# Kernel optimization log

Measured on AMD Instinct MI355X. Metric: run time of the kernel, lower is better.

Reference implementation:

```python
import jax, jax.numpy as jnp
import numpy as np

CAPACITY_FACTOR = 1.25
TOP_K = 2


def setup_inputs() -> dict:
    key = jax.random.key(0)
    ks = jax.random.split(key, 4)
    B, T, D, H, N = 8, 8192, 512, 512, 32
    x = jax.random.normal(ks[0], (B, T, D), jnp.float32)
    Wg = jax.random.normal(ks[1], (D, N), jnp.float32) * 0.02   # gate (no bias)
    W1 = jax.random.normal(ks[2], (N, D, H), jnp.float32) * 0.02  # stacked expert fc1
    b1 = jnp.zeros((N, H), jnp.float32)
    W2 = jax.random.normal(ks[3], (N, H, D), jnp.float32) * 0.02  # stacked expert fc2
    b2 = jnp.zeros((N, D), jnp.float32)
    return {"x": x, "Wg": Wg, "W1": W1, "b1": b1, "W2": W2, "b2": b2}


def _moe(x, Wg, W1, b1, W2, b2):
    B, T, D = x.shape
    N = Wg.shape[1]
    K = TOP_K
    BT = B * T
    BTK = BT * K
    C = int(np.ceil(CAPACITY_FACTOR * BTK / N))  # capacity per expert (static)

    x_flat = x.reshape(BT, D)
    probs = jax.nn.softmax(x_flat @ Wg, axis=-1)            # [BT, N]
    vals, idx = jax.lax.top_k(probs, K)                     # [BT, K]
    vals = vals / jnp.clip(vals.sum(-1, keepdims=True), 1e-9)  # normalize_gates

    # Assignments in the exact order of the original double loop: pos-major, j-minor.
    a = idx.reshape(BTK)                                    # expert id per assignment
    oh = jax.nn.one_hot(a, N, dtype=jnp.int32)              # [BTK, N]
    rank = jnp.cumsum(oh, axis=0) - oh                      # prior count for each expert
    pos = jnp.take_along_axis(rank, a[:, None], axis=1)[:, 0]  # slot within expert
    keep = pos < C                                          # capacity-limited dispatch
    dest = jnp.where(keep, a * C + pos, N * C)              # OOB sentinel -> dropped
    token = jnp.arange(BTK) // K                            # source token per assignment

    # Dispatch: scatter kept tokens into per-expert capacity buffers [N, C, D].
    buf = jnp.zeros((N * C, D), x.dtype).at[dest].set(x_flat[token], mode="drop")
    buf = buf.reshape(N, C, D)

    # Expert FFN (grouped GEMMs). FeedForwardExpert assumed Linear-ReLU-Linear.
    h = jax.nn.relu(jnp.einsum("ncd,ndh->nch", buf, W1) + b1[:, None, :])
    o = (jnp.einsum("nch,nhd->ncd", h, W2) + b2[:, None, :]).reshape(N * C, D)

    # Combine: gather expert outputs, weight by gates, scatter-add back by token.
    gathered = o[jnp.minimum(dest, N * C - 1)]              # dropped rows zeroed via w
    w = vals.reshape(BTK) * keep.astype(x.dtype)
    y_flat = jax.ops.segment_sum(gathered * w[:, None], token, num_segments=BT)
    contrib = jax.ops.segment_sum(w, token, num_segments=BT)
    # Tokens with no surviving assignment pass through unchanged.
    y_flat = jnp.where(contrib[:, None] <= 1e-12, x_flat, y_flat)
    return y_flat.reshape(B, T, D)


def reference(x, Wg, W1, b1, W2, b2):
    return _moe(x, Wg, W1, b1, W2, b2)
```

## Files before the change

### kernel.cpp

```cpp
#include <hip/hip_runtime.h>
#include <hip/hip_bf16.h>

#define BT 65536
#define DD 512
#define HH 512
#define NE 32
#define CAP 5120
#define BM 64
#define NRB 80

typedef float  f32x4  __attribute__((ext_vector_type(4)));
typedef short  bf16x8 __attribute__((ext_vector_type(8)));

__device__ __forceinline__ unsigned short f2bf(float f){
    unsigned int u = __builtin_bit_cast(unsigned int, f);
    unsigned int r = (u + 0x7fffu + ((u >> 16) & 1u)) >> 16;
    return (unsigned short)r;
}
__device__ __forceinline__ float bf2f(unsigned short h){
    unsigned int u = ((unsigned int)h) << 16;
    return __builtin_bit_cast(float, u);
}

__global__ __launch_bounds__(256) void k_wgprep(
    const float* __restrict__ Wg,
    unsigned short* __restrict__ WgHf, unsigned short* __restrict__ WgLf)
{
    int entry = blockIdx.x * 256 + threadIdx.x;
    int ln = entry & 63;
    unsigned short h[8], l[8];
    #pragma unroll
    for (int j = 0; j < 8; j++){
        int d = ((entry >> 6) & 15)*32 + (ln >> 4)*8 + j;
        int e = (entry >> 10)*16 + (ln & 15);
        float v = Wg[d*NE + e];
        unsigned short hi = f2bf(v);
        h[j] = hi;
        l[j] = f2bf(v - bf2f(hi));
    }
    *(bf16x8*)(WgHf + (size_t)entry*8) = *(bf16x8*)h;
    *(bf16x8*)(WgLf + (size_t)entry*8) = *(bf16x8*)l;
}

__global__ __launch_bounds__(256) void k_prep(
    const float* __restrict__ x, const float* __restrict__ Wg,
    const float* __restrict__ W1, const float* __restrict__ W2,
    const unsigned short* __restrict__ WgHf, const unsigned short* __restrict__ WgLf,
    unsigned short* __restrict__ W1f, unsigned short* __restrict__ W2f,
    int* __restrict__ counts, int* __restrict__ gsl, float* __restrict__ wts,
    unsigned char* __restrict__ flags, unsigned short* __restrict__ xb16)
{
    __shared__ float lg2[64 * 33];
    __shared__ int lcnt[NE], lbase[NE];

    int tid = threadIdx.x;

    if (blockIdx.x >= 1024){
        int b = blockIdx.x - 1024;
        int w = b >> 8;
        int e = (b >> 3) & 31;
        int kq = b & 7;
        const float* src = (w ? W2 : W1) + ((size_t)e << 18);
        unsigned short* dst = (w ? W2f : W1f) + ((size_t)e << 18);
        int n4 = (tid & 127) * 4;
        int kh = tid >> 7;
        #pragma unroll 1
        for (int kg = 0; kg < 4; kg++){
            int k0 = kq*64 + (kg*2 + kh)*8;
            float4 rows[8];
            #pragma unroll
            for (int j = 0; j < 8; j++)
                rows[j] = *(const float4*)&src[(size_t)(k0 + j)*512 + n4];
            unsigned short v0[8], v1[8], v2[8], v3[8];
            #pragma unroll
            for (int j = 0; j < 8; j++){
                v0[j] = f2bf(rows[j].x); v1[j] = f2bf(rows[j].y);
                v2[j] = f2bf(rows[j].z); v3[j] = f2bf(rows[j].w);
            }
            int kc = k0 >> 5, lb = ((k0 >> 3) & 3)*16;
            #pragma unroll
            for (int m = 0; m < 4; m++){
                int n = n4 + m;
                int nt = n >> 4, ln = lb + (n & 15);
                const unsigned short* vv = (m==0)?v0:(m==1)?v1:(m==2)?v2:v3;
                *(bf16x8*)(dst + (((size_t)(nt*16 + kc)*64 + ln) << 3)) = *(const bf16x8*)vv;
            }
        }
        return;
    }

    int t0 = blockIdx.x * 64;
    {
        int lane = tid & 63;
        int wv   = tid >> 6;
        int lg   = lane >> 4, ll = lane & 15;
        int tokl = wv*16 + ll;
        const float* xr = x + (size_t)(t0 + tokl)*DD;

        f32x4 acc0 = (f32x4)0.f, acc1 = (f32x4)0.f;
        #pragma unroll 4
        for (int kc = 0; kc < 16; kc++){
            int d0 = kc*32 + lg*8;
            float4 a = *(const float4*)(xr + d0);
            float4 b = *(const float4*)(xr + d0 + 4);
            unsigned short h[8], l[8];
            h[0]=f2bf(a.x); h[1]=f2bf(a.y); h[2]=f2bf(a.z); h[3]=f2bf(a.w);
            h[4]=f2bf(b.x); h[5]=f2bf(b.y); h[6]=f2bf(b.z); h[7]=f2bf(b.w);
            l[0]=f2bf(a.x-bf2f(h[0])); l[1]=f2bf(a.y-bf2f(h[1]));
            l[2]=f2bf(a.z-bf2f(h[2])); l[3]=f2bf(a.w-bf2f(h[3]));
            l[4]=f2bf(b.x-bf2f(h[4])); l[5]=f2bf(b.y-bf2f(h[5]));
            l[6]=f2bf(b.z-bf2f(h[6])); l[7]=f2bf(b.w-bf2f(h[7]));
            bf16x8 bh = *(bf16x8*)h, bl = *(bf16x8*)l;
            *(bf16x8*)(xb16 + (size_t)(t0 + tokl)*DD + d0) = bh;
            bf16x8 ah0 = *(const bf16x8*)(WgHf + ((size_t)(kc*64 + lane) << 3));
            bf16x8 al0 = *(const bf16x8*)(WgLf + ((size_t)(kc*64 + lane) << 3));
            bf16x8 ah1 = *(const bf16x8*)(WgHf + ((size_t)(1024 + kc*64 + lane) << 3));
            bf16x8 al1 = *(const bf16x8*)(WgLf + ((size_t)(1024 + kc*64 + lane) << 3));
            acc0 = __builtin_amdgcn_mfma_f32_16x16x32_bf16(ah0, bh, acc0, 0, 0, 0);
            acc0 = __builtin_amdgcn_mfma_f32_16x16x32_bf16(ah0, bl, acc0, 0, 0, 0);
            acc0 = __builtin_amdgcn_mfma_f32_16x16x32_bf16(al0, bh, acc0, 0, 0, 0);
            acc1 = __builtin_amdgcn_mfma_f32_16x16x32_bf16(ah1, bh, acc1, 0, 0, 0);
            acc1 = __builtin_amdgcn_mfma_f32_16x16x32_bf16(ah1, bl, acc1, 0, 0, 0);
            acc1 = __builtin_amdgcn_mfma_f32_16x16x32_bf16(al1, bh, acc1, 0, 0, 0);
        }
        #pragma unroll
        for (int i = 0; i < 4; i++){
            lg2[tokl*33 +      lg*4 + i] = acc0[i];
            lg2[tokl*33 + 16 + lg*4 + i] = acc1[i];
        }
    }
    if (tid < NE) lcnt[tid] = 0;
    __syncthreads();

    float w1 = 0.f, w2 = 0.f;
    int i1 = 0, i2 = 0, s1 = 0, s2 = 0;
    bool act = (tid < 64);
    if (act){
        int tok = t0 + tid;
        float acc[NE];
        #pragma unroll
        for (int n = 0; n < NE; n++) acc[n] = lg2[tid*33 + n];

        float v1 = -1e30f; i1 = -1;
        #pragma unroll
        for (int n = 0; n < NE; n++) if (acc[n] > v1){ v1 = acc[n]; i1 = n; }
        float v2 = -1e30f; i2 = -1;
        #pragma unroll
        for (int n = 0; n < NE; n++) if (n != i1 && acc[n] > v2){ v2 = acc[n]; i2 = n; }
        float v3 = -1e30f;
        #pragma unroll
        for (int n = 0; n < NE; n++) if (n != i1 && n != i2 && acc[n] > v3) v3 = acc[n];

        if (v2 - v3 >= 1e-4f){
            double ex  = exp((double)v2 - (double)v1);
            double inv = 1.0 / (1.0 + ex);
            w1 = (float)inv; w2 = (float)(ex * inv);
        } else {
            const float* xr = x + (size_t)tok * DD;
            float thresh = v2 - 1e-3f;
            unsigned cmask = 0u;
            #pragma unroll
            for (int n = 0; n < NE; n++) cmask |= (acc[n] >= thresh) ? (1u << n) : 0u;
            double dv1 = -1.0e300, dv2 = -1.0e300; int di1 = -1, di2 = -1;
            #pragma unroll 1
            for (int n = 0; n < NE; n++){
                if (!((cmask >> n) & 1u)) continue;
                double q0 = 0.0, q1 = 0.0, q2 = 0.0, q3 = 0.0;
                #pragma unroll 4
                for (int d = 0; d < DD; d += 4){
                    q0 = fma((double)xr[d+0], (double)Wg[(size_t)(d+0)*NE + n], q0);
                    q1 = fma((double)xr[d+1], (double)Wg[(size_t)(d+1)*NE + n], q1);
                    q2 = fma((double)xr[d+2], (double)Wg[(size_t)(d+2)*NE + n], q2);
                    q3 = fma((double)xr[d+3], (double)Wg[(size_t)(d+3)*NE + n], q3);
                }
                double sv = (q0 + q1) + (q2 + q3);
                if (sv > dv1){ dv2 = dv1; di2 = di1; dv1 = sv; di1 = n; }
                else if (sv > dv2){ dv2 = sv; di2 = n; }
            }
            i1 = di1; i2 = di2;
            double ex  = exp(dv2 - dv1);
            double inv = 1.0 / (1.0 + ex);
            w1 = (float)inv; w2 = (float)(ex * inv);
        }
        s1 = atomicAdd(&lcnt[i1], 1);
        s2 = atomicAdd(&lcnt[i2], 1);
    }
    __syncthreads();
    if (tid < NE && lcnt[tid] > 0) lbase[tid] = atomicAdd(&counts[tid], lcnt[tid]);
    __syncthreads();
    if (act){
        int tok = t0 + tid;
        int g1 = lbase[i1] + s1;
        int g2 = lbase[i2] + s2;
        bool k1 = g1 < CAP, k2 = g2 < CAP;
        if (k1){ gsl[i1*CAP + g1] = tok;               wts[i1*CAP + g1] = w1; }
        if (k2){ gsl[i2*CAP + g2] = tok | (1 << 20);   wts[i2*CAP + g2] = w2; }
        flags[tok] = (unsigned char)((k1 ? 1 : 0) | (k2 ? 2 : 0));
    }
}

__global__ __launch_bounds__(512, 4) void k_ffn(
    const unsigned short* __restrict__ xb16,
    const unsigned short* __restrict__ W1f,
    const unsigned short* __restrict__ W2f,
    const float* __restrict__ b1, const float* __restrict__ b2,
    const int* __restrict__ counts,
    const int* __restrict__ gsl, const float* __restrict__ wts,
    float* __restrict__ y, unsigned short* __restrict__ y2h)
{
    __shared__ unsigned char AH[64 * 1024];

    int p  = blockIdx.x;
    int s  = p >> 3;
    int e  = ((s / NRB) << 3) | (p & 7);
    int rb = s % NRB;

    int cnt = counts[e]; if (cnt > CAP) cnt = CAP;
    int r0 = rb * BM;
    if (r0 >= cnt) return;

    int tid  = threadIdx.x;
    int lane = tid & 63;
    int wv   = tid >> 6;
    int lg   = lane >> 4;
    int ll   = lane & 15;

    {
        int row = tid >> 3, seg = tid & 7;
        int gr  = r0 + row;
        char* rowb = (char*)AH + row * 1024;
        int rsw = (row & 7) << 4;
        if (gr < cnt){
            int tk = gsl[e*CAP + gr] & 0xFFFFF;
            const uint4* src = (const uint4*)(xb16 + (size_t)tk*DD + seg*64);
            #pragma unroll
            for (int j = 0; j < 8; j++){
                uint4 v = src[j];
                int chunk = seg*8 + j;
                *(uint4*)(rowb + ((chunk << 4) ^ rsw)) = v;
            }
        } else {
            uint4 zz; zz.x = zz.y = zz.z = zz.w = 0u;
            #pragma unroll
            for (int j = 0; j < 8; j++){
                int chunk = seg*8 + j;
                *(uint4*)(rowb + ((chunk << 4) ^ rsw)) = zz;
            }
        }
    }
    __syncthreads();

    f32x4 acc[4][4];
    #pragma unroll
    for (int a2 = 0; a2 < 4; a2++)
        #pragma unroll
        for (int tt = 0; tt < 4; tt++)
            acc[a2][tt] = (f32x4)0.f;

    {
        const unsigned short* Wa = W1f + ((size_t)e << 18) + (size_t)wv*32768;
        bf16x8 f0[4], f1[4];
        #pragma unroll
        for (int a2 = 0; a2 < 4; a2++)
            f0[a2] = *(const bf16x8*)(Wa + a2*8192 + lane*8);
        #pragma unroll 1
        for (int c = 0; c < 16; c += 2){
            #pragma unroll
            for (int a2 = 0; a2 < 4; a2++)
                f1[a2] = *(const bf16x8*)(Wa + a2*8192 + (c+1)*512 + lane*8);
            {
                bf16x8 bx[4];
                #pragma unroll
                for (int tt = 0; tt < 4; tt++){
                    int tok = tt*16 + ll;
                    int bofs = (64*c + 16*lg) ^ ((tok & 7) << 4);
                    bx[tt] = *(const bf16x8*)((char*)AH + tok*1024 + bofs);
                }
                __builtin_amdgcn_s_setprio(1);
                #pragma unroll
                for (int a2 = 0; a2 < 4; a2++)
                    #pragma unroll
                    for (int tt = 0; tt < 4; tt++)
                        acc[a2][tt] = __builtin_amdgcn_mfma_f32_16x16x32_bf16(f0[a2], bx[tt], acc[a2][tt], 0, 0, 0);
                __builtin_amdgcn_s_setprio(0);
            }
            if (c + 2 < 16){
                #pragma unroll
                for (int a2 = 0; a2 < 4; a2++)
                    f0[a2] = *(const bf16x8*)(Wa + a2*8192 + (c+2)*512 + lane*8);
            }
            {
                bf16x8 bx[4];
                #pragma unroll
                for (int tt = 0; tt < 4; tt++){
                    int tok = tt*16 + ll;
                    int bofs = (64*(c+1) + 16*lg) ^ ((tok & 7) << 4);
                    bx[tt] = *(const bf16x8*)((char*)AH + tok*1024 + bofs);
                }
                __builtin_amdgcn_s_setprio(1);
                #pragma unroll
                for (int a2 = 0; a2 < 4; a2++)
                    #pragma unroll
                    for (int tt = 0; tt < 4; tt++)
                        acc[a2][tt] = __builtin_amdgcn_mfma_f32_16x16x32_bf16(f1[a2], bx[tt], acc[a2][tt], 0, 0, 0);
                __builtin_amdgcn_s_setprio(0);
            }
        }
    }
    __syncthreads();

    #pragma unroll
    for (int a2 = 0; a2 < 4; a2++){
        int n0 = wv*64 + a2*16 + lg*4;
        float4 bv = *(const float4*)(b1 + e*HH + n0);
        #pragma unroll
        for (int tt = 0; tt < 4; tt++){
            int tok = tt*16 + ll;
            float h0 = acc[a2][tt][0] + bv.x; h0 = h0 > 0.f ? h0 : 0.f;
            float h1 = acc[a2][tt][1] + bv.y; h1 = h1 > 0.f ? h1 : 0.f;
            float h2 = acc[a2][tt][2] + bv.z; h2 = h2 > 0.f ? h2 : 0.f;
            float h3 = acc[a2][tt][3] + bv.w; h3 = h3 > 0.f ? h3 : 0.f;
            uint2 pk;
            pk.x = (unsigned)f2bf(h0) | ((unsigned)f2bf(h1) << 16);
            pk.y = (unsigned)f2bf(h2) | ((unsigned)f2bf(h3) << 16);
            int bofs = (n0*2) ^ ((tok & 7) << 4);
            *(uint2*)((char*)AH + tok*1024 + bofs) = pk;
            acc[a2][tt] = (f32x4)0.f;
        }
    }
    __syncthreads();

    {
        const unsigned short* Wb = W2f + ((size_t)e << 18) + (size_t)wv*32768;
        bf16x8 f0[4], f1[4];
        #pragma unroll
        for (int b_ = 0; b_ < 4; b_++)
            f0[b_] = *(const bf16x8*)(Wb + b_*8192 + lane*8);
        #pragma unroll 1
        for (int kc = 0; kc < 16; kc += 2){
            #pragma unroll
            for (int b_ = 0; b_ < 4; b_++)
                f1[b_] = *(const bf16x8*)(Wb + b_*8192 + (kc+1)*512 + lane*8);
            {
                bf16x8 ah[4];
                #pragma unroll
                for (int tt = 0; tt < 4; tt++){
                    int tok = tt*16 + ll;
                    int bofs = (64*kc + 16*lg) ^ ((tok & 7) << 4);
                    ah[tt] = *(const bf16x8*)((char*)AH + tok*1024 + bofs);
                }
                __builtin_amdgcn_s_setprio(1);
                #pragma unroll
                for (int b_ = 0; b_ < 4; b_++)
                    #pragma unroll
                    for (int tt = 0; tt < 4; tt++)
                        acc[b_][tt] = __builtin_amdgcn_mfma_f32_16x16x32_bf16(ah[tt], f0[b_], acc[b_][tt], 0, 0, 0);
                __builtin_amdgcn_s_setprio(0);
            }
            if (kc + 2 < 16){
                #pragma unroll
                for (int b_ = 0; b_ < 4; b_++)
                    f0[b_] = *(const bf16x8*)(Wb + b_*8192 + (kc+2)*512 + lane*8);
            }
            {
                bf16x8 ah[4];
                #pragma unroll
                for (int tt = 0; tt < 4; tt++){
                    int tok = tt*16 + ll;
                    int bofs = (64*(kc+1) + 16*lg) ^ ((tok & 7) << 4);
                    ah[tt] = *(const bf16x8*)((char*)AH + tok*1024 + bofs);
                }
                __builtin_amdgcn_s_setprio(1);
                #pragma unroll
                for (int b_ = 0; b_ < 4; b_++)
                    #pragma unroll
                    for (int tt = 0; tt < 4; tt++)
                        acc[b_][tt] = __builtin_amdgcn_mfma_f32_16x16x32_bf16(ah[tt], f1[b_], acc[b_][tt], 0, 0, 0);
                __builtin_amdgcn_s_setprio(0);
            }
        }
    }

    float bb[4];
    #pragma unroll
    for (int b_ = 0; b_ < 4; b_++)
        bb[b_] = b2[e*DD + wv*64 + b_*16 + ll];

    #pragma unroll
    for (int tt = 0; tt < 4; tt++){
        #pragma unroll
        for (int i = 0; i < 4; i++){
            int rl = tt*16 + lg*4 + i;
            int gr = r0 + rl;
            if (gr < cnt){
                int   v  = gsl[e*CAP + gr];
                int   tk = v & 0xFFFFF;
                float w  = wts[e*CAP + gr];
                if (v >> 20){
                    unsigned short* dst = y2h + (size_t)tk * DD;
                    #pragma unroll
                    for (int b_ = 0; b_ < 4; b_++){
                        int col = wv*64 + b_*16 + ll;
                        dst[col] = f2bf(w * (acc[b_][tt][i] + bb[b_]));
                    }
                } else {
                    float* dst = y + (size_t)tk * DD;
                    #pragma unroll
                    for (int b_ = 0; b_ < 4; b_++){
                        int col = wv*64 + b_*16 + ll;
                        dst[col] = w * (acc[b_][tt][i] + bb[b_]);
                    }
                }
            }
        }
    }
}

__global__ __launch_bounds__(256) void k_comb(
    const float* __restrict__ x, const unsigned short* __restrict__ y2h,
    const unsigned char* __restrict__ flags, float* __restrict__ y)
{
    const float4* x4  = (const float4*)x;
    const uint2*  y24 = (const uint2*)y2h;
    float4* y4 = (float4*)y;
    int nthreads = gridDim.x * 256;
    int g = blockIdx.x * 256 + threadIdx.x;
    #pragma unroll 1
    for (long long idx = g; idx < (long long)BT * 128; idx += nthreads){
        int t = (int)(idx >> 7);
        int f = flags[t];
        if (f == 3){
            float4 a = y4[idx];
            uint2 p = y24[idx];
            a.x += bf2f((unsigned short)(p.x & 0xFFFF));
            a.y += bf2f((unsigned short)(p.x >> 16));
            a.z += bf2f((unsigned short)(p.y & 0xFFFF));
            a.w += bf2f((unsigned short)(p.y >> 16));
            y4[idx] = a;
        } else if (f == 2){
            uint2 p = y24[idx];
            float4 a;
            a.x = bf2f((unsigned short)(p.x & 0xFFFF));
            a.y = bf2f((unsigned short)(p.x >> 16));
            a.z = bf2f((unsigned short)(p.y & 0xFFFF));
            a.w = bf2f((unsigned short)(p.y >> 16));
            y4[idx] = a;
        } else if (f == 0){
            y4[idx] = x4[idx];
        }
    }
}

extern "C" void kernel_launch(void* const* d_in, const int* in_sizes, int n_in,
                              void* d_out, int out_size, void* d_ws, size_t ws_size,
                              hipStream_t stream)
{
    const float* x  = (const float*)d_in[0];
    const float* Wg = (const float*)d_in[1];
    const float* W1 = (const float*)d_in[2];
    const float* b1 = (const float*)d_in[3];
    const float* W2 = (const float*)d_in[4];
    const float* b2 = (const float*)d_in[5];
    float* y = (float*)d_out;

    char* ws = (char*)d_ws;
    unsigned short* W1f = (unsigned short*)(ws);
    unsigned short* W2f = (unsigned short*)(ws + 16777216);
    size_t b3 = 33554432;
    int*   counts = (int*)  (ws + b3);
    int*   gsl    = (int*)  (ws + b3 + 256);
    float* wts    = (float*)(ws + b3 + 256 + 655360);
    unsigned char* flags = (unsigned char*)(ws + b3 + 256 + 2*655360);
    unsigned short* WgHf = (unsigned short*)(ws + b3 + 256 + 2*655360 + 65536);
    unsigned short* WgLf = (unsigned short*)(ws + b3 + 256 + 2*655360 + 65536 + 32768);
    unsigned short* xb16 = (unsigned short*)(ws + 35651584);
    unsigned short* y2h  = (unsigned short*)(ws + 35651584 + 67108864);

    hipMemsetAsync(counts, 0, 256, stream);
    hipLaunchKernelGGL(k_wgprep, dim3(8), dim3(256), 0, stream, Wg, WgHf, WgLf);
    hipLaunchKernelGGL(k_prep, dim3(1024 + 512), dim3(256), 0, stream,
                       x, Wg, W1, W2, WgHf, WgLf, W1f, W2f, counts, gsl, wts, flags, xb16);
    hipLaunchKernelGGL(k_ffn,  dim3(NE*NRB), dim3(512), 0, stream,
                       xb16, W1f, W2f, b1, b2, counts, gsl, wts, y, y2h);
    hipLaunchKernelGGL(k_comb, dim3(2048), dim3(256), 0, stream, x, y2h, flags, y);
}
```

Measured before the change: 356.1 us.

## Split prep into conversion and gating kernels; deepen FFN weight prefetch pipeline

The combined prep kernel is split in two. A conversion kernel casts the expert weights and the x-to-bf16 copy, and a separate gating kernel handles routing only, so the gate loop no longer stores xb16. In the FFN kernel the weight fragments are now prefetched four k-chunks ahead in named registers instead of double-buffered one step ahead, and launch bounds drop from 4 to 3 waves per SIMD to make room for the larger register budget. The deeper prefetch is meant to hide global-load latency behind MFMA work. The costs are one extra kernel launch, an extra full read of x, and lower occupancy.

Measured after the change: 444.5 us. +24.8%, slower.

```diff
diff --git a/kernel.cpp b/kernel.cpp
--- a/kernel.cpp
+++ b/kernel.cpp
@@ -42,21 +42,15 @@
     *(bf16x8*)(WgLf + (size_t)entry*8) = *(bf16x8*)l;
 }
 
-__global__ __launch_bounds__(256) void k_prep(
-    const float* __restrict__ x, const float* __restrict__ Wg,
+__global__ __launch_bounds__(256) void k_conv(
+    const float* __restrict__ x,
     const float* __restrict__ W1, const float* __restrict__ W2,
-    const unsigned short* __restrict__ WgHf, const unsigned short* __restrict__ WgLf,
     unsigned short* __restrict__ W1f, unsigned short* __restrict__ W2f,
-    int* __restrict__ counts, int* __restrict__ gsl, float* __restrict__ wts,
-    unsigned char* __restrict__ flags, unsigned short* __restrict__ xb16)
-{
-    __shared__ float lg2[64 * 33];
-    __shared__ int lcnt[NE], lbase[NE];
-
+    unsigned short* __restrict__ xb16)
+{
     int tid = threadIdx.x;
-
-    if (blockIdx.x >= 1024){
-        int b = blockIdx.x - 1024;
+    if (blockIdx.x < 512){
+        int b = blockIdx.x;
         int w = b >> 8;
         int e = (b >> 3) & 31;
         int kq = b & 7;
@@ -86,9 +80,34 @@
                 *(bf16x8*)(dst + (((size_t)(nt*16 + kc)*64 + ln) << 3)) = *(const bf16x8*)vv;
             }
         }
-        return;
-    }
-
+    } else {
+        int b = blockIdx.x - 512;
+        size_t base = (size_t)b * 65536;
+        const float* xs = x + base;
+        unsigned short* xd = xb16 + base;
+        #pragma unroll 1
+        for (int i = 0; i < 32; i++){
+            int o = (i*256 + tid)*8;
+            float4 a = *(const float4*)(xs + o);
+            float4 c = *(const float4*)(xs + o + 4);
+            bf16x8 pk;
+            pk[0]=(short)f2bf(a.x); pk[1]=(short)f2bf(a.y); pk[2]=(short)f2bf(a.z); pk[3]=(short)f2bf(a.w);
+            pk[4]=(short)f2bf(c.x); pk[5]=(short)f2bf(c.y); pk[6]=(short)f2bf(c.z); pk[7]=(short)f2bf(c.w);
+            *(bf16x8*)(xd + o) = pk;
+        }
+    }
+}
+
+__global__ __launch_bounds__(256) void k_gate(
+    const float* __restrict__ x, const float* __restrict__ Wg,
+    const unsigned short* __restrict__ WgHf, const unsigned short* __restrict__ WgLf,
+    int* __restrict__ counts, int* __restrict__ gsl, float* __restrict__ wts,
+    unsigned char* __restrict__ flags)
+{
+    __shared__ float lg2[64 * 33];
+    __shared__ int lcnt[NE], lbase[NE];
+
+    int tid = threadIdx.x;
     int t0 = blockIdx.x * 64;
     {
         int lane = tid & 63;
@@ -111,7 +130,6 @@
             l[4]=f2bf(b.x-bf2f(h[4])); l[5]=f2bf(b.y-bf2f(h[5]));
             l[6]=f2bf(b.z-bf2f(h[6])); l[7]=f2bf(b.w-bf2f(h[7]));
             bf16x8 bh = *(bf16x8*)h, bl = *(bf16x8*)l;
-            *(bf16x8*)(xb16 + (size_t)(t0 + tokl)*DD + d0) = bh;
             bf16x8 ah0 = *(const bf16x8*)(WgHf + ((size_t)(kc*64 + lane) << 3));
             bf16x8 al0 = *(const bf16x8*)(WgLf + ((size_t)(kc*64 + lane) << 3));
             bf16x8 ah1 = *(const bf16x8*)(WgHf + ((size_t)(1024 + kc*64 + lane) << 3));
@@ -199,7 +217,63 @@
     }
 }
 
-__global__ __launch_bounds__(512, 4) void k_ffn(
+#define LW(A,B,C,D,P,CC) { \
+    A = *(const bf16x8*)((P) + (CC)*512 + lane*8); \
+    B = *(const bf16x8*)((P) + 8192 + (CC)*512 + lane*8); \
+    C = *(const bf16x8*)((P) + 16384 + (CC)*512 + lane*8); \
+    D = *(const bf16x8*)((P) + 24576 + (CC)*512 + lane*8); }
+
+#define CHUNK1(CC,A,B,C,D) { \
+    int base_ = (64*(CC) + 16*lg) ^ sw_; \
+    bf16x8 x0_ = *(const bf16x8*)((char*)AH + (ll)*1024      + base_); \
+    bf16x8 x1_ = *(const bf16x8*)((char*)AH + (16+ll)*1024   + base_); \
+    bf16x8 x2_ = *(const bf16x8*)((char*)AH + (32+ll)*1024   + base_); \
+    bf16x8 x3_ = *(const bf16x8*)((char*)AH + (48+ll)*1024   + base_); \
+    __builtin_amdgcn_s_setprio(1); \
+    acc[0][0]=__builtin_amdgcn_mfma_f32_16x16x32_bf16(A,x0_,acc[0][0],0,0,0); \
+    acc[0][1]=__builtin_amdgcn_mfma_f32_16x16x32_bf16(A,x1_,acc[0][1],0,0,0); \
+    acc[0][2]=__builtin_amdgcn_mfma_f32_16x16x32_bf16(A,x2_,acc[0][2],0,0,0); \
+    acc[0][3]=__builtin_amdgcn_mfma_f32_16x16x32_bf16(A,x3_,acc[0][3],0,0,0); \
+    acc[1][0]=__builtin_amdgcn_mfma_f32_16x16x32_bf16(B,x0_,acc[1][0],0,0,0); \
+    acc[1][1]=__builtin_amdgcn_mfma_f32_16x16x32_bf16(B,x1_,acc[1][1],0,0,0); \
+    acc[1][2]=__builtin_amdgcn_mfma_f32_16x16x32_bf16(B,x2_,acc[1][2],0,0,0); \
+    acc[1][3]=__builtin_amdgcn_mfma_f32_16x16x32_bf16(B,x3_,acc[1][3],0,0,0); \
+    acc[2][0]=__builtin_amdgcn_mfma_f32_16x16x32_bf16(C,x0_,acc[2][0],0,0,0); \
+    acc[2][1]=__builtin_amdgcn_mfma_f32_16x16x32_bf16(C,x1_,acc[2][1],0,0,0); \
+    acc[2][2]=__builtin_amdgcn_mfma_f32_16x16x32_bf16(C,x2_,acc[2][2],0,0,0); \
+    acc[2][3]=__builtin_amdgcn_mfma_f32_16x16x32_bf16(C,x3_,acc[2][3],0,0,0); \
+    acc[3][0]=__builtin_amdgcn_mfma_f32_16x16x32_bf16(D,x0_,acc[3][0],0,0,0); \
+    acc[3][1]=__builtin_amdgcn_mfma_f32_16x16x32_bf16(D,x1_,acc[3][1],0,0,0); \
+    acc[3][2]=__builtin_amdgcn_mfma_f32_16x16x32_bf16(D,x2_,acc[3][2],0,0,0); \
+    acc[3][3]=__builtin_amdgcn_mfma_f32_16x16x32_bf16(D,x3_,acc[3][3],0,0,0); \
+    __builtin_amdgcn_s_setprio(0); }
+
+#define CHUNK2(CC,A,B,C,D) { \
+    int base_ = (64*(CC) + 16*lg) ^ sw_; \
+    bf16x8 x0_ = *(const bf16x8*)((char*)AH + (ll)*1024      + base_); \
+    bf16x8 x1_ = *(const bf16x8*)((char*)AH + (16+ll)*1024   + base_); \
+    bf16x8 x2_ = *(const bf16x8*)((char*)AH + (32+ll)*1024   + base_); \
+    bf16x8 x3_ = *(const bf16x8*)((char*)AH + (48+ll)*1024   + base_); \
+    __builtin_amdgcn_s_setprio(1); \
+    acc[0][0]=__builtin_amdgcn_mfma_f32_16x16x32_bf16(x0_,A,acc[0][0],0,0,0); \
+    acc[0][1]=__builtin_amdgcn_mfma_f32_16x16x32_bf16(x1_,A,acc[0][1],0,0,0); \
+    acc[0][2]=__builtin_amdgcn_mfma_f32_16x16x32_bf16(x2_,A,acc[0][2],0,0,0); \
+    acc[0][3]=__builtin_amdgcn_mfma_f32_16x16x32_bf16(x3_,A,acc[0][3],0,0,0); \
+    acc[1][0]=__builtin_amdgcn_mfma_f32_16x16x32_bf16(x0_,B,acc[1][0],0,0,0); \
+    acc[1][1]=__builtin_amdgcn_mfma_f32_16x16x32_bf16(x1_,B,acc[1][1],0,0,0); \
+    acc[1][2]=__builtin_amdgcn_mfma_f32_16x16x32_bf16(x2_,B,acc[1][2],0,0,0); \
+    acc[1][3]=__builtin_amdgcn_mfma_f32_16x16x32_bf16(x3_,B,acc[1][3],0,0,0); \
+    acc[2][0]=__builtin_amdgcn_mfma_f32_16x16x32_bf16(x0_,C,acc[2][0],0,0,0); \
+    acc[2][1]=__builtin_amdgcn_mfma_f32_16x16x32_bf16(x1_,C,acc[2][1],0,0,0); \
+    acc[2][2]=__builtin_amdgcn_mfma_f32_16x16x32_bf16(x2_,C,acc[2][2],0,0,0); \
+    acc[2][3]=__builtin_amdgcn_mfma_f32_16x16x32_bf16(x3_,C,acc[2][3],0,0,0); \
+    acc[3][0]=__builtin_amdgcn_mfma_f32_16x16x32_bf16(x0_,D,acc[3][0],0,0,0); \
+    acc[3][1]=__builtin_amdgcn_mfma_f32_16x16x32_bf16(x1_,D,acc[3][1],0,0,0); \
+    acc[3][2]=__builtin_amdgcn_mfma_f32_16x16x32_bf16(x2_,D,acc[3][2],0,0,0); \
+    acc[3][3]=__builtin_amdgcn_mfma_f32_16x16x32_bf16(x3_,D,acc[3][3],0,0,0); \
+    __builtin_amdgcn_s_setprio(0); }
+
+__global__ __launch_bounds__(512, 3) void k_ffn(
     const unsigned short* __restrict__ xb16,
     const unsigned short* __restrict__ W1f,
     const unsigned short* __restrict__ W2f,
@@ -224,6 +298,7 @@
     int wv   = tid >> 6;
     int lg   = lane >> 4;
     int ll   = lane & 15;
+    int sw_  = (ll & 7) << 4;
 
     {
         int row = tid >> 3, seg = tid & 7;
@@ -259,52 +334,21 @@
 
     {
         const unsigned short* Wa = W1f + ((size_t)e << 18) + (size_t)wv*32768;
-        bf16x8 f0[4], f1[4];
-        #pragma unroll
-        for (int a2 = 0; a2 < 4; a2++)
-            f0[a2] = *(const bf16x8*)(Wa + a2*8192 + lane*8);
+        bf16x8 q0a,q0b,q0c,q0d, q1a,q1b,q1c,q1d, q2a,q2b,q2c,q2d, q3a,q3b,q3c,q3d;
+        LW(q0a,q0b,q0c,q0d,Wa,0)
+        LW(q1a,q1b,q1c,q1d,Wa,1)
+        LW(q2a,q2b,q2c,q2d,Wa,2)
+        LW(q3a,q3b,q3c,q3d,Wa,3)
         #pragma unroll 1
-        for (int c = 0; c < 16; c += 2){
-            #pragma unroll
-            for (int a2 = 0; a2 < 4; a2++)
-                f1[a2] = *(const bf16x8*)(Wa + a2*8192 + (c+1)*512 + lane*8);
-            {
-                bf16x8 bx[4];
-                #pragma unroll
-                for (int tt = 0; tt < 4; tt++){
-                    int tok = tt*16 + ll;
-                    int bofs = (64*c + 16*lg) ^ ((tok & 7) << 4);
-                    bx[tt] = *(const bf16x8*)((char*)AH + tok*1024 + bofs);
-                }
-                __builtin_amdgcn_s_setprio(1);
-                #pragma unroll
-                for (int a2 = 0; a2 < 4; a2++)
-                    #pragma unroll
-                    for (int tt = 0; tt < 4; tt++)
-                        acc[a2][tt] = __builtin_amdgcn_mfma_f32_16x16x32_bf16(f0[a2], bx[tt], acc[a2][tt], 0, 0, 0);
-                __builtin_amdgcn_s_setprio(0);
-            }
-            if (c + 2 < 16){
-                #pragma unroll
-                for (int a2 = 0; a2 < 4; a2++)
-                    f0[a2] = *(const bf16x8*)(Wa + a2*8192 + (c+2)*512 + lane*8);
-            }
-            {
-                bf16x8 bx[4];
-                #pragma unroll
-                for (int tt = 0; tt < 4; tt++){
-                    int tok = tt*16 + ll;
-                    int bofs = (64*(c+1) + 16*lg) ^ ((tok & 7) << 4);
-                    bx[tt] = *(const bf16x8*)((char*)AH + tok*1024 + bofs);
-                }
-                __builtin_amdgcn_s_setprio(1);
-                #pragma unroll
-                for (int a2 = 0; a2 < 4; a2++)
-                    #pragma unroll
-                    for (int tt = 0; tt < 4; tt++)
-                        acc[a2][tt] = __builtin_amdgcn_mfma_f32_16x16x32_bf16(f1[a2], bx[tt], acc[a2][tt], 0, 0, 0);
-                __builtin_amdgcn_s_setprio(0);
-            }
+        for (int c = 0; c < 16; c += 4){
+            CHUNK1(c,   q0a,q0b,q0c,q0d)
+            if (c+4 < 16) LW(q0a,q0b,q0c,q0d,Wa,c+4)
+            CHUNK1(c+1, q1a,q1b,q1c,q1d)
+            if (c+5 < 16) LW(q1a,q1b,q1c,q1d,Wa,c+5)
+            CHUNK1(c+2, q2a,q2b,q2c,q2d)
+            if (c+6 < 16) LW(q2a,q2b,q2c,q2d,Wa,c+6)
+            CHUNK1(c+3, q3a,q3b,q3c,q3d)
+            if (c+7 < 16) LW(q3a,q3b,q3c,q3d,Wa,c+7)
         }
     }
     __syncthreads();
@@ -332,52 +376,21 @@
 
     {
         const unsigned short* Wb = W2f + ((size_t)e << 18) + (size_t)wv*32768;
-        bf16x8 f0[4], f1[4];
-        #pragma unroll
-        for (int b_ = 0; b_ < 4; b_++)
-            f0[b_] = *(const bf16x8*)(Wb + b_*8192 + lane*8);
+        bf16x8 q0a,q0b,q0c,q0d, q1a,q1b,q1c,q1d, q2a,q2b,q2c,q2d, q3a,q3b,q3c,q3d;
+        LW(q0a,q0b,q0c,q0d,Wb,0)
+        LW(q1a,q1b,q1c,q1d,Wb,1)
+        LW(q2a,q2b,q2c,q2d,Wb,2)
+        LW(q3a,q3b,q3c,q3d,Wb,3)
         #pragma unroll 1
-        for (int kc = 0; kc < 16; kc += 2){
-            #pragma unroll
-            for (int b_ = 0; b_ < 4; b_++)
-                f1[b_] = *(const bf16x8*)(Wb + b_*8192 + (kc+1)*512 + lane*8);
-            {
-                bf16x8 ah[4];
-                #pragma unroll
-                for (int tt = 0; tt < 4; tt++){
-                    int tok = tt*16 + ll;
-                    int bofs = (64*kc + 16*lg) ^ ((tok & 7) << 4);
-                    ah[tt] = *(const bf16x8*)((char*)AH + tok*1024 + bofs);
-                }
-                __builtin_amdgcn_s_setprio(1);
-                #pragma unroll
-                for (int b_ = 0; b_ < 4; b_++)
-                    #pragma unroll
-                    for (int tt = 0; tt < 4; tt++)
-                        acc[b_][tt] = __builtin_amdgcn_mfma_f32_16x16x32_bf16(ah[tt], f0[b_], acc[b_][tt], 0, 0, 0);
-                __builtin_amdgcn_s_setprio(0);
-            }
-            if (kc + 2 < 16){
-                #pragma unroll
-                for (int b_ = 0; b_ < 4; b_++)
-                    f0[b_] = *(const bf16x8*)(Wb + b_*8192 + (kc+2)*512 + lane*8);
-            }
-            {
-                bf16x8 ah[4];
-                #pragma unroll
-                for (int tt = 0; tt < 4; tt++){
-                    int tok = tt*16 + ll;
-                    int bofs = (64*(kc+1) + 16*lg) ^ ((tok & 7) << 4);
-                    ah[tt] = *(const bf16x8*)((char*)AH + tok*1024 + bofs);
-                }
-                __builtin_amdgcn_s_setprio(1);
-                #pragma unroll
-                for (int b_ = 0; b_ < 4; b_++)
-                    #pragma unroll
-                    for (int tt = 0; tt < 4; tt++)
-                        acc[b_][tt] = __builtin_amdgcn_mfma_f32_16x16x32_bf16(ah[tt], f1[b_], acc[b_][tt], 0, 0, 0);
-                __builtin_amdgcn_s_setprio(0);
-            }
+        for (int kc = 0; kc < 16; kc += 4){
+            CHUNK2(kc,   q0a,q0b,q0c,q0d)
+            if (kc+4 < 16) LW(q0a,q0b,q0c,q0d,Wb,kc+4)
+            CHUNK2(kc+1, q1a,q1b,q1c,q1d)
+            if (kc+5 < 16) LW(q1a,q1b,q1c,q1d,Wb,kc+5)
+            CHUNK2(kc+2, q2a,q2b,q2c,q2d)
+            if (kc+6 < 16) LW(q2a,q2b,q2c,q2d,Wb,kc+6)
+            CHUNK2(kc+3, q3a,q3b,q3c,q3d)
+            if (kc+7 < 16) LW(q3a,q3b,q3c,q3d,Wb,kc+7)
         }
     }
 
@@ -478,9 +491,8 @@
 
     hipMemsetAsync(counts, 0, 256, stream);
     hipLaunchKernelGGL(k_wgprep, dim3(8), dim3(256), 0, stream, Wg, WgHf, WgLf);
-    hipLaunchKernelGGL(k_prep, dim3(1024 + 512), dim3(256), 0, stream,
-                       x, Wg, W1, W2, WgHf, WgLf, W1f, W2f, counts, gsl, wts, flags, xb16);
-    hipLaunchKernelGGL(k_ffn,  dim3(NE*NRB), dim3(512), 0, stream,
-                       xb16, W1f, W2f, b1, b2, counts, gsl, wts, y, y2h);
+    hipLaunchKernelGGL(k_conv, dim3(1024), dim3(256), 0, stream, x, W1, W2, W1f, W2f, xb16);
+    hipLaunchKernelGGL(k_gate, dim3(BT/64), dim3(256), 0, stream, x, Wg, WgHf, WgLf, counts, gsl, wts, flags);
+    hipLaunchKernelGGL(k_ffn,  dim3(NE*NRB), dim3(512), 0, stream, xb16, W1f, W2f, b1, b2, counts, gsl, wts, y, y2h);
     hipLaunchKernelGGL(k_comb, dim3(2048), dim3(256), 0, stream, x, y2h, flags, y);
 }
```

## Split prep kernel, prefetch gate loads, write both expert outputs as bf16

Applied to the files above, without the earlier changes.

The combined prep kernel is split into a weight-conversion kernel and a gating kernel. The gate loop now prefetches the next x chunk one iteration ahead. The FFN writes the first-choice contribution to a bf16 scratch buffer instead of directly into fp32 y, and the combine kernel sums both bf16 buffers. This aims to cut scattered fp32 write traffic and hide load latency, at the cost of an extra launch, an extra buffer read in combine, and lower precision for the first-choice output.

Result: no change. 362.8 us (+1.9%).

```diff
diff --git a/kernel.cpp b/kernel.cpp
--- a/kernel.cpp
+++ b/kernel.cpp
@@ -42,11 +42,46 @@
     *(bf16x8*)(WgLf + (size_t)entry*8) = *(bf16x8*)l;
 }
 
-__global__ __launch_bounds__(256) void k_prep(
+__global__ __launch_bounds__(256) void k_wconv(
+    const float* __restrict__ W1, const float* __restrict__ W2,
+    unsigned short* __restrict__ W1f, unsigned short* __restrict__ W2f)
+{
+    int tid = threadIdx.x;
+    int b = blockIdx.x;
+    int w = b >> 8;
+    int e = (b >> 3) & 31;
+    int kq = b & 7;
+    const float* src = (w ? W2 : W1) + ((size_t)e << 18);
+    unsigned short* dst = (w ? W2f : W1f) + ((size_t)e << 18);
+    int n4 = (tid & 127) * 4;
+    int kh = tid >> 7;
+    #pragma unroll 1
+    for (int kg = 0; kg < 4; kg++){
+        int k0 = kq*64 + (kg*2 + kh)*8;
+        float4 rows[8];
+        #pragma unroll
+        for (int j = 0; j < 8; j++)
+            rows[j] = *(const float4*)&src[(size_t)(k0 + j)*512 + n4];
+        unsigned short v0[8], v1[8], v2[8], v3[8];
+        #pragma unroll
+        for (int j = 0; j < 8; j++){
+            v0[j] = f2bf(rows[j].x); v1[j] = f2bf(rows[j].y);
+            v2[j] = f2bf(rows[j].z); v3[j] = f2bf(rows[j].w);
+        }
+        int kc = k0 >> 5, lb = ((k0 >> 3) & 3)*16;
+        #pragma unroll
+        for (int m = 0; m < 4; m++){
+            int n = n4 + m;
+            int nt = n >> 4, ln = lb + (n & 15);
+            const unsigned short* vv = (m==0)?v0:(m==1)?v1:(m==2)?v2:v3;
+            *(bf16x8*)(dst + (((size_t)(nt*16 + kc)*64 + ln) << 3)) = *(const bf16x8*)vv;
+        }
+    }
+}
+
+__global__ __launch_bounds__(256) void k_gate(
     const float* __restrict__ x, const float* __restrict__ Wg,
-    const float* __restrict__ W1, const float* __restrict__ W2,
     const unsigned short* __restrict__ WgHf, const unsigned short* __restrict__ WgLf,
-    unsigned short* __restrict__ W1f, unsigned short* __restrict__ W2f,
     int* __restrict__ counts, int* __restrict__ gsl, float* __restrict__ wts,
     unsigned char* __restrict__ flags, unsigned short* __restrict__ xb16)
 {
@@ -54,41 +89,6 @@
     __shared__ int lcnt[NE], lbase[NE];
 
     int tid = threadIdx.x;
-
-    if (blockIdx.x >= 1024){
-        int b = blockIdx.x - 1024;
-        int w = b >> 8;
-        int e = (b >> 3) & 31;
-        int kq = b & 7;
-        const float* src = (w ? W2 : W1) + ((size_t)e << 18);
-        unsigned short* dst = (w ? W2f : W1f) + ((size_t)e << 18);
-        int n4 = (tid & 127) * 4;
-        int kh = tid >> 7;
-        #pragma unroll 1
-        for (int kg = 0; kg < 4; kg++){
-            int k0 = kq*64 + (kg*2 + kh)*8;
-            float4 rows[8];
-            #pragma unroll
-            for (int j = 0; j < 8; j++)
-                rows[j] = *(const float4*)&src[(size_t)(k0 + j)*512 + n4];
-            unsigned short v0[8], v1[8], v2[8], v3[8];
-            #pragma unroll
-            for (int j = 0; j < 8; j++){
-                v0[j] = f2bf(rows[j].x); v1[j] = f2bf(rows[j].y);
-                v2[j] = f2bf(rows[j].z); v3[j] = f2bf(rows[j].w);
-            }
-            int kc = k0 >> 5, lb = ((k0 >> 3) & 3)*16;
-            #pragma unroll
-            for (int m = 0; m < 4; m++){
-                int n = n4 + m;
-                int nt = n >> 4, ln = lb + (n & 15);
-                const unsigned short* vv = (m==0)?v0:(m==1)?v1:(m==2)?v2:v3;
-                *(bf16x8*)(dst + (((size_t)(nt*16 + kc)*64 + ln) << 3)) = *(const bf16x8*)vv;
-            }
-        }
-        return;
-    }
-
     int t0 = blockIdx.x * 64;
     {
         int lane = tid & 63;
@@ -98,11 +98,14 @@
         const float* xr = x + (size_t)(t0 + tokl)*DD;
 
         f32x4 acc0 = (f32x4)0.f, acc1 = (f32x4)0.f;
+        float4 pa = *(const float4*)(xr + lg*8);
+        float4 pb = *(const float4*)(xr + lg*8 + 4);
         #pragma unroll 4
         for (int kc = 0; kc < 16; kc++){
-            int d0 = kc*32 + lg*8;
-            float4 a = *(const float4*)(xr + d0);
-            float4 b = *(const float4*)(xr + d0 + 4);
+            int dn = (kc < 15) ? (kc+1)*32 + lg*8 : lg*8;
+            float4 na = *(const float4*)(xr + dn);
+            float4 nb = *(const float4*)(xr + dn + 4);
+            float4 a = pa, b = pb;
             unsigned short h[8], l[8];
             h[0]=f2bf(a.x); h[1]=f2bf(a.y); h[2]=f2bf(a.z); h[3]=f2bf(a.w);
             h[4]=f2bf(b.x); h[5]=f2bf(b.y); h[6]=f2bf(b.z); h[7]=f2bf(b.w);
@@ -111,7 +114,7 @@
             l[4]=f2bf(b.x-bf2f(h[4])); l[5]=f2bf(b.y-bf2f(h[5]));
             l[6]=f2bf(b.z-bf2f(h[6])); l[7]=f2bf(b.w-bf2f(h[7]));
             bf16x8 bh = *(bf16x8*)h, bl = *(bf16x8*)l;
-            *(bf16x8*)(xb16 + (size_t)(t0 + tokl)*DD + d0) = bh;
+            *(bf16x8*)(xb16 + (size_t)(t0 + tokl)*DD + kc*32 + lg*8) = bh;
             bf16x8 ah0 = *(const bf16x8*)(WgHf + ((size_t)(kc*64 + lane) << 3));
             bf16x8 al0 = *(const bf16x8*)(WgLf + ((size_t)(kc*64 + lane) << 3));
             bf16x8 ah1 = *(const bf16x8*)(WgHf + ((size_t)(1024 + kc*64 + lane) << 3));
@@ -122,6 +125,7 @@
             acc1 = __builtin_amdgcn_mfma_f32_16x16x32_bf16(ah1, bh, acc1, 0, 0, 0);
             acc1 = __builtin_amdgcn_mfma_f32_16x16x32_bf16(ah1, bl, acc1, 0, 0, 0);
             acc1 = __builtin_amdgcn_mfma_f32_16x16x32_bf16(al1, bh, acc1, 0, 0, 0);
+            pa = na; pb = nb;
         }
         #pragma unroll
         for (int i = 0; i < 4; i++){
@@ -206,7 +210,7 @@
     const float* __restrict__ b1, const float* __restrict__ b2,
     const int* __restrict__ counts,
     const int* __restrict__ gsl, const float* __restrict__ wts,
-    float* __restrict__ y, unsigned short* __restrict__ y2h)
+    unsigned short* __restrict__ y1h, unsigned short* __restrict__ y2h)
 {
     __shared__ unsigned char AH[64 * 1024];
 
@@ -396,20 +400,11 @@
                 int   v  = gsl[e*CAP + gr];
                 int   tk = v & 0xFFFFF;
                 float w  = wts[e*CAP + gr];
-                if (v >> 20){
-                    unsigned short* dst = y2h + (size_t)tk * DD;
-                    #pragma unroll
-                    for (int b_ = 0; b_ < 4; b_++){
-                        int col = wv*64 + b_*16 + ll;
-                        dst[col] = f2bf(w * (acc[b_][tt][i] + bb[b_]));
-                    }
-                } else {
-                    float* dst = y + (size_t)tk * DD;
-                    #pragma unroll
-                    for (int b_ = 0; b_ < 4; b_++){
-                        int col = wv*64 + b_*16 + ll;
-                        dst[col] = w * (acc[b_][tt][i] + bb[b_]);
-                    }
+                unsigned short* dst = ((v >> 20) ? y2h : y1h) + (size_t)tk * DD;
+                #pragma unroll
+                for (int b_ = 0; b_ < 4; b_++){
+                    int col = wv*64 + b_*16 + ll;
+                    dst[col] = f2bf(w * (acc[b_][tt][i] + bb[b_]));
                 }
             }
         }
@@ -417,10 +412,12 @@
 }
 
 __global__ __launch_bounds__(256) void k_comb(
-    const float* __restrict__ x, const unsigned short* __restrict__ y2h,
+    const float* __restrict__ x, const unsigned short* __restrict__ y1h,
+    const unsigned short* __restrict__ y2h,
     const unsigned char* __restrict__ flags, float* __restrict__ y)
 {
     const float4* x4  = (const float4*)x;
+    const uint2*  y14 = (const uint2*)y1h;
     const uint2*  y24 = (const uint2*)y2h;
     float4* y4 = (float4*)y;
     int nthreads = gridDim.x * 256;
@@ -429,25 +426,26 @@
     for (long long idx = g; idx < (long long)BT * 128; idx += nthreads){
         int t = (int)(idx >> 7);
         int f = flags[t];
-        if (f == 3){
-            float4 a = y4[idx];
-            uint2 p = y24[idx];
-            a.x += bf2f((unsigned short)(p.x & 0xFFFF));
-            a.y += bf2f((unsigned short)(p.x >> 16));
-            a.z += bf2f((unsigned short)(p.y & 0xFFFF));
-            a.w += bf2f((unsigned short)(p.y >> 16));
-            y4[idx] = a;
-        } else if (f == 2){
-            uint2 p = y24[idx];
-            float4 a;
-            a.x = bf2f((unsigned short)(p.x & 0xFFFF));
-            a.y = bf2f((unsigned short)(p.x >> 16));
-            a.z = bf2f((unsigned short)(p.y & 0xFFFF));
-            a.w = bf2f((unsigned short)(p.y >> 16));
-            y4[idx] = a;
-        } else if (f == 0){
-            y4[idx] = x4[idx];
-        }
+        float4 a; a.x = a.y = a.z = a.w = 0.f;
+        if (f == 0){
+            a = x4[idx];
+        } else {
+            if (f & 1){
+                uint2 p = y14[idx];
+                a.x += bf2f((unsigned short)(p.x & 0xFFFF));
+                a.y += bf2f((unsigned short)(p.x >> 16));
+                a.z += bf2f((unsigned short)(p.y & 0xFFFF));
+                a.w += bf2f((unsigned short)(p.y >> 16));
+            }
+            if (f & 2){
+                uint2 p = y24[idx];
+                a.x += bf2f((unsigned short)(p.x & 0xFFFF));
+                a.y += bf2f((unsigned short)(p.x >> 16));
+                a.z += bf2f((unsigned short)(p.y & 0xFFFF));
+                a.w += bf2f((unsigned short)(p.y >> 16));
+            }
+        }
+        y4[idx] = a;
     }
 }
 
@@ -475,12 +473,14 @@
     unsigned short* WgLf = (unsigned short*)(ws + b3 + 256 + 2*655360 + 65536 + 32768);
     unsigned short* xb16 = (unsigned short*)(ws + 35651584);
     unsigned short* y2h  = (unsigned short*)(ws + 35651584 + 67108864);
+    unsigned short* y1h  = (unsigned short*)(ws + 35651584 + 2ull*67108864);
 
     hipMemsetAsync(counts, 0, 256, stream);
     hipLaunchKernelGGL(k_wgprep, dim3(8), dim3(256), 0, stream, Wg, WgHf, WgLf);
-    hipLaunchKernelGGL(k_prep, dim3(1024 + 512), dim3(256), 0, stream,
-                       x, Wg, W1, W2, WgHf, WgLf, W1f, W2f, counts, gsl, wts, flags, xb16);
+    hipLaunchKernelGGL(k_wconv, dim3(512), dim3(256), 0, stream, W1, W2, W1f, W2f);
+    hipLaunchKernelGGL(k_gate, dim3(BT/64), dim3(256), 0, stream,
+                       x, Wg, WgHf, WgLf, counts, gsl, wts, flags, xb16);
     hipLaunchKernelGGL(k_ffn,  dim3(NE*NRB), dim3(512), 0, stream,
-                       xb16, W1f, W2f, b1, b2, counts, gsl, wts, y, y2h);
-    hipLaunchKernelGGL(k_comb, dim3(2048), dim3(256), 0, stream, x, y2h, flags, y);
-}
+                       xb16, W1f, W2f, b1, b2, counts, gsl, wts, y1h, y2h);
+    hipLaunchKernelGGL(k_comb, dim3(2048), dim3(256), 0, stream, x, y1h, y2h, flags, y);
+}
```
